# Optimization experiments

Hardware: AMD Instinct MI355X
Metric: run time of the kernel (lower is better)

The kernel has to match this reference:

```python
import jax, jax.numpy as jnp
import numpy as np

KERNEL_MUL = 2.0
KERNEL_NUM = 5


def _mmd(source, target):
    n = source.shape[0]
    total = jnp.concatenate([source, target], axis=0)          # [2N, D]
    n_samples = total.shape[0]
    # GEMM-based pairwise squared L2 distances (same math as broadcast subtract/square/sum)
    sq = jnp.sum(total * total, axis=-1)                        # [2N]
    L2 = sq[:, None] + sq[None, :] - 2.0 * (total @ total.T)    # [2N, 2N]
    # bandwidth from detached distances (torch uses .data)
    bw = jax.lax.stop_gradient(jnp.sum(L2)) / (n_samples ** 2 - n_samples)
    bw = bw / (KERNEL_MUL ** (KERNEL_NUM // 2))
    kernels = jnp.zeros_like(L2)
    for i in range(KERNEL_NUM):
        kernels = kernels + jnp.exp(-L2 / (bw * KERNEL_MUL ** i))
    XX = kernels[:n, :n]
    YY = kernels[n:, n:]
    XY = kernels[:n, n:]
    YX = kernels[n:, :n]
    return jnp.mean(XX + YY - XY - YX)


def setup_inputs() -> dict:
    key = jax.random.key(0)
    k1, k2 = jax.random.split(key)
    N, D = 4096, 128
    source = jax.random.normal(k1, (N, D), dtype=jnp.float32)
    target = jax.random.normal(k2, (N, D), dtype=jnp.float32)
    return {"source": source, "target": target}


def reference(source, target):
    return _mmd(source, target)
```

## Files before the change

### kernel.cpp

```cpp
#include <hip/hip_runtime.h>

#define D 128
#define NT64 8256

typedef __attribute__((ext_vector_type(8))) short short8;
typedef __attribute__((ext_vector_type(4))) float float4v;

static __device__ __forceinline__ unsigned short f2bf(float f) {
    unsigned int u = __float_as_uint(f);
    unsigned int r = (u + 0x7fffu + ((u >> 16) & 1u)) >> 16;
    return (unsigned short)r;
}


__global__ __launch_bounds__(256) void k_prep(const float* __restrict__ src,
                                              const float* __restrict__ tgt,
                                              float* __restrict__ wsf,
                                              unsigned int* __restrict__ XTu) {
    if (blockIdx.x < 2048) {
        float* rowsq = wsf + 33280;
        const int wv = threadIdx.x >> 6, lane = threadIdx.x & 63;
        const int gr = blockIdx.x * 4 + wv;
        const float* Xr = (gr < 4096) ? src + (size_t)gr * D : tgt + (size_t)(gr - 4096) * D;
        float2 f = ((const float2*)Xr)[lane];
        XTu[(gr >> 4) * 1024 + (lane >> 2) * 64 + (gr & 15) * 4 + (lane & 3)] =
            (unsigned)f2bf(f.x) | ((unsigned)f2bf(f.y) << 16);
        float s = f.x * f.x + f.y * f.y;
        #pragma unroll
        for (int off = 32; off; off >>= 1) s += __shfl_down(s, off);
        if (lane == 0) rowsq[gr] = s;
    } else {
        float* colpart = wsf + 512;
        int b = blockIdx.x - 2048;
        int col = threadIdx.x & 127, half = threadIdx.x >> 7;
        const float* X = (b < 64) ? src + (size_t)(b * 64) * D
                                  : tgt + (size_t)((b - 64) * 64) * D;
        float p0 = 0.f, p1 = 0.f, p2 = 0.f, p3 = 0.f;
        #pragma unroll 4
        for (int i = 0; i < 32; i += 4) {
            p0 += X[(size_t)(2 * (i + 0) + half) * D + col];
            p1 += X[(size_t)(2 * (i + 1) + half) * D + col];
            p2 += X[(size_t)(2 * (i + 2) + half) * D + col];
            p3 += X[(size_t)(2 * (i + 3) + half) * D + col];
        }
        __shared__ float cp[2][128];
        cp[half][col] = (p0 + p1) + (p2 + p3);
        __syncthreads();
        if (threadIdx.x < 128)
            colpart[b * 128 + threadIdx.x] = cp[0][threadIdx.x] + cp[1][threadIdx.x];
    }
}

__global__ __launch_bounds__(256) void p3_consts(float* __restrict__ wsf) {
    const float* colpart = wsf + 512;
    const float* rowsq = wsf + 33280;
    const int tid = threadIdx.x, lane = tid & 63;

    float s0 = 0.f, s1 = 0.f, s2 = 0.f, s3 = 0.f;
    #pragma unroll
    for (int i = 0; i < 32; i += 4) {
        s0 += rowsq[tid + 256 * (i + 0)];
        s1 += rowsq[tid + 256 * (i + 1)];
        s2 += rowsq[tid + 256 * (i + 2)];
        s3 += rowsq[tid + 256 * (i + 3)];
    }
    float s = (s0 + s1) + (s2 + s3);
    #pragma unroll
    for (int off = 32; off; off >>= 1) s += __shfl_down(s, off);
    __shared__ float red[8];
    __shared__ float csum[128];
    if (lane == 0) red[tid >> 6] = s;

    int c = tid & 127, h = tid >> 7;
    float q0 = 0.f, q1 = 0.f, q2 = 0.f, q3 = 0.f;
    #pragma unroll 4
    for (int b = 0; b < 64; b += 4) {
        q0 += colpart[(h * 64 + b + 0) * 128 + c];
        q1 += colpart[(h * 64 + b + 1) * 128 + c];
        q2 += colpart[(h * 64 + b + 2) * 128 + c];
        q3 += colpart[(h * 64 + b + 3) * 128 + c];
    }
    float cs = (q0 + q1) + (q2 + q3);
    __syncthreads();
    if (h == 0) csum[c] = cs;
    __syncthreads();
    if (h == 1) csum[c] += cs;
    __syncthreads();
    float v = (tid < 128) ? csum[tid] * csum[tid] : 0.f;
    #pragma unroll
    for (int off = 32; off; off >>= 1) v += __shfl_down(v, off);
    if (lane == 0) red[4 + (tid >> 6)] = v;
    __syncthreads();
    if (tid == 0) {
        double ss = (double)red[0] + red[1] + red[2] + red[3];
        double s2 = (double)red[4] + red[5] + red[6] + red[7];
        double sumL2 = 2.0 * 8192.0 * ss - 2.0 * s2;
        double bw = sumL2 / (8192.0 * 8192.0 - 8192.0) / 4.0;
        wsf[4] = (float)(-1.4426950408889634 / (bw * 16.0));
    }
}

__global__ __launch_bounds__(256, 4) void mmd_main(const uint4* __restrict__ XT,
                                                   const float* __restrict__ wsf,
                                                   float* __restrict__ partial) {
    const float* rowsq = wsf + 33280;
    const int lane = threadIdx.x & 63, wv = threadIdx.x >> 6;
    const int quad = lane >> 4, mrow = lane & 15;

    int t = blockIdx.x * 4 + wv;
    int ti = (int)((257.0 - sqrt(257.0 * 257.0 - 8.0 * (double)t)) * 0.5);
    auto base = [](int b) { return (b * (257 - b)) >> 1; };
    while (base(ti + 1) <= t) ++ti;
    while (base(ti) > t) --ti;
    int tj = ti + (t - base(ti));

    const uint4* A = XT + (size_t)ti * 1024;
    const uint4* B = XT + (size_t)tj * 1024;
    float c4 = wsf[4];

    float4v acc[4][4];
    #pragma unroll
    for (int mt = 0; mt < 4; ++mt)
        #pragma unroll
        for (int nt = 0; nt < 4; ++nt)
            acc[mt][nt] = (float4v){0.f, 0.f, 0.f, 0.f};

    #pragma unroll
    for (int kc = 0; kc < 4; ++kc) {
        short8 af[4], bf[4];
        #pragma unroll
        for (int mt = 0; mt < 4; ++mt)
            af[mt] = *(const short8*)&A[mt * 256 + kc * 64 + lane];
        #pragma unroll
        for (int nt = 0; nt < 4; ++nt)
            bf[nt] = *(const short8*)&B[nt * 256 + kc * 64 + lane];
        #pragma unroll
        for (int mt = 0; mt < 4; ++mt)
            #pragma unroll
            for (int nt = 0; nt < 4; ++nt)
                acc[mt][nt] = __builtin_amdgcn_mfma_f32_16x16x32_bf16(af[mt], bf[nt], acc[mt][nt], 0, 0, 0);
    }

    const float* rsqA = rowsq + ti * 64;
    const float* rsqB = rowsq + tj * 64;
    const float cm2 = -2.f * c4;
    float part = 0.f;
    #pragma unroll
    for (int mt = 0; mt < 4; ++mt) {
        float rAc[4];
        #pragma unroll
        for (int r = 0; r < 4; ++r) rAc[r] = rsqA[mt * 16 + quad * 4 + r] * c4;
        #pragma unroll
        for (int nt = 0; nt < 4; ++nt) {
            float rBc = rsqB[nt * 16 + mrow] * c4;
            float4v d = acc[mt][nt];
            #pragma unroll
            for (int r = 0; r < 4; ++r) {
                float e1 = __builtin_amdgcn_exp2f(__builtin_fmaf(d[r], cm2, rAc[r] + rBc));
                float e2 = e1 * e1, e4 = e2 * e2, e8 = e4 * e4, e16 = e8 * e8;
                part += ((e1 + e2) + (e4 + e8)) + e16;
            }
        }
    }
    #pragma unroll
    for (int off = 32; off; off >>= 1) part += __shfl_down(part, off);
    if (lane == 0) {
        float wgt = ((ti < 64) == (tj < 64)) ? 1.f : -1.f;
        if (ti != tj) wgt *= 2.f;
        partial[t] = wgt * part;
    }
}

__global__ __launch_bounds__(256) void f_final(const float* __restrict__ wsf,
                                               float* __restrict__ out) {
    const float* partial = wsf + 41472;
    int tid = threadIdx.x, lane = tid & 63;
    double a0 = 0.0, a1 = 0.0, a2 = 0.0, a3 = 0.0;
    #pragma unroll 4
    for (int i = tid; i < NT64; i += 1024) {
        a0 += (double)partial[i];
        if (i + 256 < NT64) a1 += (double)partial[i + 256];
        if (i + 512 < NT64) a2 += (double)partial[i + 512];
        if (i + 768 < NT64) a3 += (double)partial[i + 768];
    }
    double s = (a0 + a1) + (a2 + a3);
    #pragma unroll
    for (int off = 32; off; off >>= 1) s += __shfl_down(s, off);
    __shared__ double r4[4];
    if (lane == 0) r4[tid >> 6] = s;
    __syncthreads();
    if (tid == 0)
        out[0] = (float)(((r4[0] + r4[1]) + (r4[2] + r4[3])) * (1.0 / (4096.0 * 4096.0)));
}

extern "C" void kernel_launch(void* const* d_in, const int* in_sizes, int n_in,
                              void* d_out, int out_size, void* d_ws, size_t ws_size,
                              hipStream_t stream) {
    const float* src = (const float*)d_in[0];
    const float* tgt = (const float*)d_in[1];
    float* wsf = (float*)d_ws;
    unsigned int* XTu = (unsigned int*)(wsf + 65536);
    float* partial = wsf + 41472;

    hipLaunchKernelGGL(k_prep, dim3(2176), dim3(256), 0, stream, src, tgt, wsf, XTu);
    hipLaunchKernelGGL(p3_consts, dim3(1), dim3(256), 0, stream, wsf);
    hipLaunchKernelGGL(mmd_main, dim3(NT64 / 4), dim3(256), 0, stream,
                       (const uint4*)XTu, wsf, partial);
    hipLaunchKernelGGL(f_final, dim3(1), dim3(256), 0, stream, wsf, (float*)d_out);
}
```

Baseline: 94.65 us.

## Fuse final reduction into main kernel via atomics and pack epilogue math

Removes the separate final-reduction kernel. Each wave atomically adds its weighted partial into one of 32 double accumulators, and the last wave, found through an atomic counter, sums them and writes the output. The accumulators and counter are zeroed in the constants kernel. The epilogue exp and power arithmetic is also rewritten on float2 vectors so the compiler can emit packed FP32 ops. This saves one launch and a pass over the partial sums, at the cost of atomic contention, nondeterministic summation order and reliance on fences.

After: 230.2 us. 143% more time.

```diff
diff --git a/kernel.cpp b/kernel.cpp
--- a/kernel.cpp
+++ b/kernel.cpp
@@ -5,6 +5,7 @@
 
 typedef __attribute__((ext_vector_type(8))) short short8;
 typedef __attribute__((ext_vector_type(4))) float float4v;
+typedef __attribute__((ext_vector_type(2))) float float2v;
 
 static __device__ __forceinline__ unsigned short f2bf(float f) {
     unsigned int u = __float_as_uint(f);
@@ -56,6 +57,9 @@
     const float* rowsq = wsf + 33280;
     const int tid = threadIdx.x, lane = tid & 63;
 
+    if (tid < 32) ((double*)(wsf + 16))[tid] = 0.0;
+    if (tid == 32) ((unsigned int*)wsf)[8] = 0u;
+
     float s0 = 0.f, s1 = 0.f, s2 = 0.f, s3 = 0.f;
     #pragma unroll
     for (int i = 0; i < 32; i += 4) {
@@ -101,8 +105,8 @@
 }
 
 __global__ __launch_bounds__(256, 4) void mmd_main(const uint4* __restrict__ XT,
-                                                   const float* __restrict__ wsf,
-                                                   float* __restrict__ partial) {
+                                                   float* __restrict__ wsf,
+                                                   float* __restrict__ out) {
     const float* rowsq = wsf + 33280;
     const int lane = threadIdx.x & 63, wv = threadIdx.x >> 6;
     const int quad = lane >> 4, mrow = lane & 15;
@@ -144,53 +148,50 @@
     const float* rsqA = rowsq + ti * 64;
     const float* rsqB = rowsq + tj * 64;
     const float cm2 = -2.f * c4;
-    float part = 0.f;
+    const float2v cm2v = {cm2, cm2};
+    float2v part2 = {0.f, 0.f};
     #pragma unroll
     for (int mt = 0; mt < 4; ++mt) {
-        float rAc[4];
-        #pragma unroll
-        for (int r = 0; r < 4; ++r) rAc[r] = rsqA[mt * 16 + quad * 4 + r] * c4;
+        const float2v rA01 = { rsqA[mt * 16 + quad * 4 + 0] * c4,
+                               rsqA[mt * 16 + quad * 4 + 1] * c4 };
+        const float2v rA23 = { rsqA[mt * 16 + quad * 4 + 2] * c4,
+                               rsqA[mt * 16 + quad * 4 + 3] * c4 };
         #pragma unroll
         for (int nt = 0; nt < 4; ++nt) {
             float rBc = rsqB[nt * 16 + mrow] * c4;
+            const float2v rB2 = {rBc, rBc};
             float4v d = acc[mt][nt];
-            #pragma unroll
-            for (int r = 0; r < 4; ++r) {
-                float e1 = __builtin_amdgcn_exp2f(__builtin_fmaf(d[r], cm2, rAc[r] + rBc));
-                float e2 = e1 * e1, e4 = e2 * e2, e8 = e4 * e4, e16 = e8 * e8;
-                part += ((e1 + e2) + (e4 + e8)) + e16;
-            }
+            float2v d01 = {d[0], d[1]}, d23 = {d[2], d[3]};
+            float2v a01 = d01 * cm2v + (rA01 + rB2);
+            float2v a23 = d23 * cm2v + (rA23 + rB2);
+            float2v e1a = { __builtin_amdgcn_exp2f(a01[0]), __builtin_amdgcn_exp2f(a01[1]) };
+            float2v e1b = { __builtin_amdgcn_exp2f(a23[0]), __builtin_amdgcn_exp2f(a23[1]) };
+            float2v e2a = e1a * e1a, e4a = e2a * e2a, e8a = e4a * e4a, e16a = e8a * e8a;
+            float2v e2b = e1b * e1b, e4b = e2b * e2b, e8b = e4b * e4b, e16b = e8b * e8b;
+            part2 += (e1a + e2a) + ((e4a + e8a) + e16a);
+            part2 += (e1b + e2b) + ((e4b + e8b) + e16b);
         }
     }
+    float part = part2[0] + part2[1];
     #pragma unroll
     for (int off = 32; off; off >>= 1) part += __shfl_down(part, off);
+
     if (lane == 0) {
         float wgt = ((ti < 64) == (tj < 64)) ? 1.f : -1.f;
         if (ti != tj) wgt *= 2.f;
-        partial[t] = wgt * part;
-    }
-}
-
-__global__ __launch_bounds__(256) void f_final(const float* __restrict__ wsf,
-                                               float* __restrict__ out) {
-    const float* partial = wsf + 41472;
-    int tid = threadIdx.x, lane = tid & 63;
-    double a0 = 0.0, a1 = 0.0, a2 = 0.0, a3 = 0.0;
-    #pragma unroll 4
-    for (int i = tid; i < NT64; i += 1024) {
-        a0 += (double)partial[i];
-        if (i + 256 < NT64) a1 += (double)partial[i + 256];
-        if (i + 512 < NT64) a2 += (double)partial[i + 512];
-        if (i + 768 < NT64) a3 += (double)partial[i + 768];
-    }
-    double s = (a0 + a1) + (a2 + a3);
-    #pragma unroll
-    for (int off = 32; off; off >>= 1) s += __shfl_down(s, off);
-    __shared__ double r4[4];
-    if (lane == 0) r4[tid >> 6] = s;
-    __syncthreads();
-    if (tid == 0)
-        out[0] = (float)(((r4[0] + r4[1]) + (r4[2] + r4[3])) * (1.0 / (4096.0 * 4096.0)));
+        double* accd = (double*)(wsf + 16);
+        unsigned int* cnt = ((unsigned int*)wsf) + 8;
+        atomicAdd(accd + (t & 31), (double)(wgt * part));
+        __threadfence();
+        unsigned int old = atomicAdd(cnt, 1u);
+        if (old == NT64 - 1) {
+            __threadfence();
+            double s = 0.0;
+            #pragma unroll
+            for (int i = 0; i < 32; ++i) s += atomicAdd(accd + i, 0.0);
+            out[0] = (float)(s * (1.0 / (4096.0 * 4096.0)));
+        }
+    }
 }
 
 extern "C" void kernel_launch(void* const* d_in, const int* in_sizes, int n_in,
@@ -200,11 +201,9 @@
     const float* tgt = (const float*)d_in[1];
     float* wsf = (float*)d_ws;
     unsigned int* XTu = (unsigned int*)(wsf + 65536);
-    float* partial = wsf + 41472;
 
     hipLaunchKernelGGL(k_prep, dim3(2176), dim3(256), 0, stream, src, tgt, wsf, XTu);
     hipLaunchKernelGGL(p3_consts, dim3(1), dim3(256), 0, stream, wsf);
     hipLaunchKernelGGL(mmd_main, dim3(NT64 / 4), dim3(256), 0, stream,
-                       (const uint4*)XTu, wsf, partial);
-    hipLaunchKernelGGL(f_final, dim3(1), dim3(256), 0, stream, wsf, (float*)d_out);
-}
+                       (const uint4*)XTu, wsf, (float*)d_out);
+}
```

## Stage 128-row tile pairs in LDS via async global-to-LDS loads with packed FP32 epilogue

Applied to the files above, without the earlier changes.

Each block now computes a 128x128 tile pair, with four waves sharing A and B panels staged in LDS through global_load_lds. Before, each wave loaded its own 64x64 operands straight from global memory. The change cuts redundant global/L2 traffic, and the exp/sum epilogue is rewritten with float2 vectors to encourage packed FP32 math. Blockswizzling spreads the tile pairs across XCDs. In exchange it uses 64KB of LDS per block, which lowers occupancy, adds a block barrier, and wastes one wave's work on diagonal tiles (weight zero).

Result: no change. 93.11 us (-1.6%).

```diff
diff --git a/kernel.cpp b/kernel.cpp
--- a/kernel.cpp
+++ b/kernel.cpp
@@ -1,15 +1,23 @@
 #include <hip/hip_runtime.h>
 
 #define D 128
-#define NT64 8256
+#define NT2 2080
+#define NPART 8320
 
 typedef __attribute__((ext_vector_type(8))) short short8;
 typedef __attribute__((ext_vector_type(4))) float float4v;
+typedef __attribute__((ext_vector_type(2))) float float2v;
 
 static __device__ __forceinline__ unsigned short f2bf(float f) {
     unsigned int u = __float_as_uint(f);
     unsigned int r = (u + 0x7fffu + ((u >> 16) & 1u)) >> 16;
     return (unsigned short)r;
+}
+
+static __device__ __forceinline__ void gld16(const void* g, void* l) {
+    __builtin_amdgcn_global_load_lds(
+        (const __attribute__((address_space(1))) unsigned int*)g,
+        (__attribute__((address_space(3))) unsigned int*)l, 16, 0, 0);
 }
 
 
@@ -100,23 +108,41 @@
     }
 }
 
-__global__ __launch_bounds__(256, 4) void mmd_main(const uint4* __restrict__ XT,
-                                                   const float* __restrict__ wsf,
-                                                   float* __restrict__ partial) {
+__global__ __launch_bounds__(256) void mmd_main(const uint4* __restrict__ XT,
+                                                const float* __restrict__ wsf,
+                                                float* __restrict__ partial) {
+    __shared__ uint4 lds[4096];
     const float* rowsq = wsf + 33280;
-    const int lane = threadIdx.x & 63, wv = threadIdx.x >> 6;
+    const int tid = threadIdx.x;
+    const int lane = tid & 63, wv = tid >> 6;
     const int quad = lane >> 4, mrow = lane & 15;
-
-    int t = blockIdx.x * 4 + wv;
-    int ti = (int)((257.0 - sqrt(257.0 * 257.0 - 8.0 * (double)t)) * 0.5);
-    auto base = [](int b) { return (b * (257 - b)) >> 1; };
-    while (base(ti + 1) <= t) ++ti;
-    while (base(ti) > t) --ti;
-    int tj = ti + (t - base(ti));
-
-    const uint4* A = XT + (size_t)ti * 1024;
-    const uint4* B = XT + (size_t)tj * 1024;
+    const int wm = wv >> 1, wn = wv & 1;
+
+    int b = blockIdx.x;
+    int t2 = (b & 7) * (NT2 / 8) + (b >> 3);
+
+    int pi = (int)((129.0 - sqrt(129.0 * 129.0 - 8.0 * (double)t2)) * 0.5);
+    auto base = [](int p) { return (p * (129 - p)) >> 1; };
+    while (base(pi + 1) <= t2) ++pi;
+    while (base(pi) > t2) --pi;
+    int pj = pi + (t2 - base(pi));
+
+    const char* gA = (const char*)(XT + (size_t)pi * 2048);
+    char* lb = (char*)lds;
+    #pragma unroll
+    for (int it = 0; it < 8; ++it)
+        gld16(gA + it * 4096 + tid * 16, lb + it * 4096 + tid * 16);
+    if (pj != pi) {
+        const char* gB = (const char*)(XT + (size_t)pj * 2048);
+        #pragma unroll
+        for (int it = 0; it < 8; ++it)
+            gld16(gB + it * 4096 + tid * 16, lb + 32768 + it * 4096 + tid * 16);
+    }
+    const uint4* As = lds + wm * 1024;
+    const uint4* Bs = ((pj != pi) ? lds + 2048 : lds) + wn * 1024;
+    const int ti = pi * 2 + wm, tj = pj * 2 + wn;
     float c4 = wsf[4];
+    __syncthreads();
 
     float4v acc[4][4];
     #pragma unroll
@@ -130,10 +156,10 @@
         short8 af[4], bf[4];
         #pragma unroll
         for (int mt = 0; mt < 4; ++mt)
-            af[mt] = *(const short8*)&A[mt * 256 + kc * 64 + lane];
+            af[mt] = *(const short8*)&As[mt * 256 + kc * 64 + lane];
         #pragma unroll
         for (int nt = 0; nt < 4; ++nt)
-            bf[nt] = *(const short8*)&B[nt * 256 + kc * 64 + lane];
+            bf[nt] = *(const short8*)&Bs[nt * 256 + kc * 64 + lane];
         #pragma unroll
         for (int mt = 0; mt < 4; ++mt)
             #pragma unroll
@@ -144,30 +170,43 @@
     const float* rsqA = rowsq + ti * 64;
     const float* rsqB = rowsq + tj * 64;
     const float cm2 = -2.f * c4;
-    float part = 0.f;
+    const float2v cm2v = {cm2, cm2};
+    float2v part2 = {0.f, 0.f};
     #pragma unroll
     for (int mt = 0; mt < 4; ++mt) {
-        float rAc[4];
-        #pragma unroll
-        for (int r = 0; r < 4; ++r) rAc[r] = rsqA[mt * 16 + quad * 4 + r] * c4;
+        const float2v rA01 = { rsqA[mt * 16 + quad * 4 + 0] * c4,
+                               rsqA[mt * 16 + quad * 4 + 1] * c4 };
+        const float2v rA23 = { rsqA[mt * 16 + quad * 4 + 2] * c4,
+                               rsqA[mt * 16 + quad * 4 + 3] * c4 };
         #pragma unroll
         for (int nt = 0; nt < 4; ++nt) {
             float rBc = rsqB[nt * 16 + mrow] * c4;
+            const float2v rB2 = {rBc, rBc};
             float4v d = acc[mt][nt];
-            #pragma unroll
-            for (int r = 0; r < 4; ++r) {
-                float e1 = __builtin_amdgcn_exp2f(__builtin_fmaf(d[r], cm2, rAc[r] + rBc));
-                float e2 = e1 * e1, e4 = e2 * e2, e8 = e4 * e4, e16 = e8 * e8;
-                part += ((e1 + e2) + (e4 + e8)) + e16;
-            }
+            float2v d01 = {d[0], d[1]}, d23 = {d[2], d[3]};
+            float2v a01 = d01 * cm2v + (rA01 + rB2);
+            float2v a23 = d23 * cm2v + (rA23 + rB2);
+            float2v e1a = { __builtin_amdgcn_exp2f(a01[0]), __builtin_amdgcn_exp2f(a01[1]) };
+            float2v e1b = { __builtin_amdgcn_exp2f(a23[0]), __builtin_amdgcn_exp2f(a23[1]) };
+            float2v e2a = e1a * e1a, e4a = e2a * e2a, e8a = e4a * e4a, e16a = e8a * e8a;
+            float2v e2b = e1b * e1b, e4b = e2b * e2b, e8b = e4b * e4b, e16b = e8b * e8b;
+            part2 += (e1a + e2a) + ((e4a + e8a) + e16a);
+            part2 += (e1b + e2b) + ((e4b + e8b) + e16b);
         }
     }
+    float part = part2[0] + part2[1];
     #pragma unroll
     for (int off = 32; off; off >>= 1) part += __shfl_down(part, off);
+
     if (lane == 0) {
-        float wgt = ((ti < 64) == (tj < 64)) ? 1.f : -1.f;
-        if (ti != tj) wgt *= 2.f;
-        partial[t] = wgt * part;
+        float wgt;
+        if (pi == pj) {
+            if (wm == 1 && wn == 0) wgt = 0.f;
+            else wgt = (ti == tj) ? 1.f : 2.f;
+        } else {
+            wgt = ((pi < 32) == (pj < 32)) ? 2.f : -2.f;
+        }
+        partial[t2 * 4 + wv] = wgt * part;
     }
 }
 
@@ -177,11 +216,11 @@
     int tid = threadIdx.x, lane = tid & 63;
     double a0 = 0.0, a1 = 0.0, a2 = 0.0, a3 = 0.0;
     #pragma unroll 4
-    for (int i = tid; i < NT64; i += 1024) {
+    for (int i = tid; i < NPART; i += 1024) {
         a0 += (double)partial[i];
-        if (i + 256 < NT64) a1 += (double)partial[i + 256];
-        if (i + 512 < NT64) a2 += (double)partial[i + 512];
-        if (i + 768 < NT64) a3 += (double)partial[i + 768];
+        if (i + 256 < NPART) a1 += (double)partial[i + 256];
+        if (i + 512 < NPART) a2 += (double)partial[i + 512];
+        if (i + 768 < NPART) a3 += (double)partial[i + 768];
     }
     double s = (a0 + a1) + (a2 + a3);
     #pragma unroll
@@ -204,7 +243,7 @@
 
     hipLaunchKernelGGL(k_prep, dim3(2176), dim3(256), 0, stream, src, tgt, wsf, XTu);
     hipLaunchKernelGGL(p3_consts, dim3(1), dim3(256), 0, stream, wsf);
-    hipLaunchKernelGGL(mmd_main, dim3(NT64 / 4), dim3(256), 0, stream,
+    hipLaunchKernelGGL(mmd_main, dim3(NT2), dim3(256), 0, stream,
                        (const uint4*)XTu, wsf, partial);
     hipLaunchKernelGGL(f_final, dim3(1), dim3(256), 0, stream, wsf, (float*)d_out);
 }
```
